# Kernel optimization log

Measured on AMD Instinct MI355X. Metric: run time of the kernel, lower is better.

## Reference

```python
import jax, jax.numpy as jnp
import numpy as np

B, L, H = 2, 2048, 2048
NH, NKV, HD = 16, 8, 128
K = 4            # conv kernel size
BASE = 1000000.0 # rotary base
H2 = NH // 2
N_REP = NH // NKV


def setup_inputs() -> dict:
    key = jax.random.key(0)
    ks = jax.random.split(key, 12)
    s = 0.02
    hidden_states = jax.random.normal(ks[0], (B, L, H), jnp.float32)
    idx = jnp.arange(L)
    diff = (idx[:, None] - idx[None, :]).astype(jnp.float32)
    # lightning-attention decay mask: -(i-j) on/below diagonal, -1e9 above
    lin_attention_mask = jnp.where(diff >= 0, -diff, -1e9).astype(jnp.float32)
    # additive causal mask for softmax half
    attention_mask = jnp.where(diff >= 0, 0.0, -1e9).astype(jnp.float32)[None, None]
    # ALiBi-style positive per-head slopes for the linear half
    slope_rate = (2.0 ** (-8.0 * jnp.arange(1, H2 + 1, dtype=jnp.float32) / H2)).reshape(H2, 1, 1)
    position_ids = jnp.arange(L, dtype=jnp.int32)
    Wq = s * jax.random.normal(ks[1], (H, H), jnp.float32)
    bq = jnp.zeros((H,), jnp.float32)
    Wk = s * jax.random.normal(ks[2], (H, NKV * HD), jnp.float32)
    bk = jnp.zeros((NKV * HD,), jnp.float32)
    Wv = s * jax.random.normal(ks[3], (H, NKV * HD), jnp.float32)
    bv = jnp.zeros((NKV * HD,), jnp.float32)
    Wo = s * jax.random.normal(ks[4], (H, H), jnp.float32)
    # conv init: identity tap at last index + tiny noise (matches _init_conv_to_one)
    q_conv_w = jnp.zeros((H // 2, K), jnp.float32).at[:, K - 1].set(1.0) + 1e-4 * jax.random.normal(ks[5], (H // 2, K), jnp.float32)
    q_conv_b = jnp.zeros((H // 2,), jnp.float32)
    k_conv_w = jnp.zeros((NKV * HD, K), jnp.float32).at[:, K - 1].set(1.0) + 1e-4 * jax.random.normal(ks[6], (NKV * HD, K), jnp.float32)
    k_conv_b = jnp.zeros((NKV * HD,), jnp.float32)
    return dict(hidden_states=hidden_states, lin_attention_mask=lin_attention_mask,
                attention_mask=attention_mask, slope_rate=slope_rate, position_ids=position_ids,
                Wq=Wq, bq=bq, Wk=Wk, bk=bk, Wv=Wv, bv=bv, Wo=Wo,
                q_conv_w=q_conv_w, q_conv_b=q_conv_b, k_conv_w=k_conv_w, k_conv_b=k_conv_b)


def _dwconv_causal(x, w, b):
    # x: [B,L,C]; w: [C,K]; b: [C]. Causal depthwise conv (torch Conv1d cross-correlation,
    # padding K-1 then truncate to first L positions).
    xp = jnp.pad(x, ((0, 0), (K - 1, 0), (0, 0)))
    y = b
    for i in range(K):
        y = y + xp[:, i:i + x.shape[1], :] * w[:, i]
    return y


def _rot_half(x):
    return jnp.concatenate([-x[..., HD // 2:], x[..., :HD // 2]], axis=-1)


def _rep_kv(x):
    # [B,NKV,L,D] -> [B,NH,L,D] via repeat_interleave on head dim
    return jnp.repeat(x, N_REP, axis=1)


def reference(hidden_states, lin_attention_mask, attention_mask, slope_rate, position_ids,
              Wq, bq, Wk, bk, Wv, bv, Wo, q_conv_w, q_conv_b, k_conv_w, k_conv_b):
    q = hidden_states @ Wq + bq          # [B,L,H]
    k = hidden_states @ Wk + bk          # [B,L,NKV*HD]
    v = hidden_states @ Wv + bv          # [B,L,NKV*HD]

    # ---- softmax half (first NH//2 heads, rotary) ----
    qs = q[..., :H // 2].reshape(B, L, H2, HD).transpose(0, 2, 1, 3)   # [B,H2,L,D]
    ks_ = k.reshape(B, L, NKV, HD).transpose(0, 2, 1, 3)               # [B,NKV,L,D]
    vs = v.reshape(B, L, NKV, HD).transpose(0, 2, 1, 3)
    inv_freq = 1.0 / (BASE ** (jnp.arange(0, HD, 2, dtype=jnp.float32) / HD))
    freqs = position_ids.astype(jnp.float32)[:, None] * inv_freq[None, :]
    emb = jnp.concatenate([freqs, freqs], axis=-1)                     # [L,D]
    cos, sin = jnp.cos(emb)[None, None], jnp.sin(emb)[None, None]
    qs = qs * cos + _rot_half(qs) * sin
    kr = ks_ * cos + _rot_half(ks_) * sin
    k_soft = _rep_kv(kr)[:, :H2]
    v_soft = _rep_kv(vs)[:, :H2]
    attn = jnp.einsum('bhnd,bhmd->bhnm', qs, k_soft) / np.sqrt(HD).astype(np.float32)
    attn = attn + attention_mask
    attn = jax.nn.softmax(attn.astype(jnp.float32), axis=-1).astype(qs.dtype)
    attn_out = jnp.einsum('bhnm,bhmd->bhnd', attn, v_soft)
    attn_out = attn_out.transpose(0, 2, 1, 3).reshape(B, L, H // 2)

    # ---- linear half (last NH//2 heads: conv -> silu -> decayed linear attention) ----
    q_tnorm = _dwconv_causal(q[..., H // 2:], q_conv_w, q_conv_b)      # [B,L,H/2]
    kc = _dwconv_causal(k, k_conv_w, k_conv_b)                          # [B,L,NKV*HD]
    qt = jax.nn.silu(q_tnorm).reshape(B, L, H2, HD).transpose(0, 2, 1, 3)
    kc = jax.nn.silu(kc).reshape(B, L, NKV, HD).transpose(0, 2, 1, 3)
    k_lin = _rep_kv(kc)[:, H2:]
    v_lin = _rep_kv(vs)[:, H2:]
    lin_mask = jnp.exp(slope_rate * lin_attention_mask)                 # [H2,L,L]
    energy = jnp.einsum('bhnd,bhmd->bhnm', qt, k_lin) * lin_mask
    out_t = jnp.einsum('bhnm,bhmd->bhnd', energy, v_lin)
    out_t = out_t.transpose(0, 2, 1, 3).reshape(B, L, H // 2)
    # SimpleRMSNorm (no weight), computed in fp32
    ot32 = out_t.astype(jnp.float32)
    out_t = (ot32 * jax.lax.rsqrt(jnp.mean(ot32 * ot32, axis=-1, keepdims=True) + 1e-6)).astype(out_t.dtype)

    return jnp.concatenate([attn_out, out_t], axis=-1) @ Wo
```

## Files before the change

kernel.cpp:

```cpp
#include <hip/hip_runtime.h>
#include <hip/hip_bf16.h>

typedef __attribute__((ext_vector_type(8))) short short8;
typedef __attribute__((ext_vector_type(4))) float f32x4;
typedef __attribute__((ext_vector_type(16))) float f32x16;

__device__ __forceinline__ void gl_lds16(const void* g, void* l) {
    void* gp = const_cast<void*>(g);
    __builtin_amdgcn_global_load_lds((__attribute__((address_space(1))) void*)gp,
                                     (__attribute__((address_space(3))) void*)l, 16, 0, 0);
}
__device__ __forceinline__ short f2bf(float f) {
    __hip_bfloat16 h = __float2bfloat16(f);
    return __builtin_bit_cast(short, h);
}
__device__ __forceinline__ float bf2f(__hip_bfloat16 h) { return __bfloat162float(h); }
__device__ __forceinline__ float bfbits2f(short s) {
    unsigned int u = ((unsigned int)(unsigned short)s) << 16;
    return __builtin_bit_cast(float, u);
}
__device__ __forceinline__ void store_val(float* C, size_t i, float v) { C[i] = v; }
__device__ __forceinline__ void store_val(__hip_bfloat16* C, size_t i, float v) { C[i] = __float2bfloat16(v); }

__global__ __launch_bounds__(256) void cast_kernel(const float* __restrict__ in, __hip_bfloat16* __restrict__ out) {
    size_t i = (size_t)blockIdx.x * 256 + threadIdx.x;
    float4 v = ((const float4*)in)[i];
    ushort4 o;
    o.x = (unsigned short)f2bf(v.x); o.y = (unsigned short)f2bf(v.y);
    o.z = (unsigned short)f2bf(v.z); o.w = (unsigned short)f2bf(v.w);
    ((ushort4*)out)[i] = o;
}

__global__ __launch_bounds__(256) void biascat_kernel(const float* __restrict__ bq, const float* __restrict__ bk,
                                                      const float* __restrict__ bv, float* __restrict__ o) {
    int i = blockIdx.x * 256 + threadIdx.x;
    o[i] = (i < 2048) ? bq[i] : ((i < 3072) ? bk[i - 2048] : bv[i - 3072]);
}

__global__ __launch_bounds__(256) void transpose_w4_kernel(
    const float* __restrict__ Wq, const float* __restrict__ Wo,
    const float* __restrict__ Wk, const float* __restrict__ Wv,
    __hip_bfloat16* __restrict__ oq, __hip_bfloat16* __restrict__ oo, __hip_bfloat16* __restrict__ okv)
{
    int z = blockIdx.z;
    const float* in; __hip_bfloat16* out; int C;
    if (z == 0)      { in = Wq; out = oq; C = 2048; }
    else if (z == 1) { in = Wo; out = oo; C = 2048; }
    else if (z == 2) { in = Wk; out = okv; C = 1024; }
    else             { in = Wv; out = okv + (size_t)1024 * 2048; C = 1024; }
    int c0 = blockIdx.x * 64, r0 = blockIdx.y * 64;
    if (c0 >= C) return;
    __shared__ float tile[64][65];
    int t = threadIdx.x, tx = t & 15, ty = t >> 4;
#pragma unroll
    for (int i = 0; i < 4; ++i) {
        float4 v = *(const float4*)(in + (size_t)(r0 + ty + i * 16) * C + c0 + tx * 4);
        tile[ty + i * 16][tx * 4 + 0] = v.x; tile[ty + i * 16][tx * 4 + 1] = v.y;
        tile[ty + i * 16][tx * 4 + 2] = v.z; tile[ty + i * 16][tx * 4 + 3] = v.w;
    }
    __syncthreads();
#pragma unroll
    for (int i = 0; i < 4; ++i) {
        int lc = ty + i * 16, lr0 = tx * 4;
        ushort4 o;
        o.x = (unsigned short)f2bf(tile[lr0 + 0][lc]);
        o.y = (unsigned short)f2bf(tile[lr0 + 1][lc]);
        o.z = (unsigned short)f2bf(tile[lr0 + 2][lc]);
        o.w = (unsigned short)f2bf(tile[lr0 + 3][lc]);
        *(ushort4*)(out + (size_t)(c0 + lc) * 2048 + r0 + lr0) = o;
    }
}

template <typename OutT, bool HAS_BIAS, bool SPLIT>
__global__ __launch_bounds__(256) void gemm_bt_kernel(
    const __hip_bfloat16* __restrict__ A, const __hip_bfloat16* __restrict__ Bt,
    const float* __restrict__ bias, OutT* __restrict__ C, OutT* __restrict__ C2,
    int M, int N, int K)
{
    __shared__ short As[128 * 64];
    __shared__ short Bs[128 * 64];
    int t = threadIdx.x, lane = t & 63, w = t >> 6;
    int m0 = blockIdx.y * 128, n0 = blockIdx.x * 128;
    int wr = (w >> 1) * 64, wc = (w & 1) * 64;
    f32x16 acc[2][2];
#pragma unroll
    for (int i = 0; i < 2; ++i)
#pragma unroll
        for (int j = 0; j < 2; ++j)
#pragma unroll
            for (int e = 0; e < 16; ++e) acc[i][j][e] = 0.f;
    int srow = w * 8 + (lane >> 3);
    int scol = ((lane & 7) ^ (lane >> 3)) * 8;
    const __hip_bfloat16* Ag = A + (size_t)(m0 + srow) * K + scol;
    const __hip_bfloat16* Bg = Bt + (size_t)(n0 + srow) * K + scol;
    short* AsB = As + w * 8 * 64;
    short* BsB = Bs + w * 8 * 64;
    int l31 = lane & 31, khalf = lane >> 5;
    for (int k0 = 0; k0 < K; k0 += 64) {
#pragma unroll
        for (int it = 0; it < 4; ++it) {
            gl_lds16(Ag + (size_t)it * 32 * K + k0, AsB + it * 32 * 64);
            gl_lds16(Bg + (size_t)it * 32 * K + k0, BsB + it * 32 * 64);
        }
        __syncthreads();
#pragma unroll
        for (int s = 0; s < 4; ++s) {
            int chunk = s * 2 + khalf;
            short8 a[2], b[2];
#pragma unroll
            for (int mi = 0; mi < 2; ++mi) {
                int row = wr + mi * 32 + l31;
                a[mi] = *(const short8*)&As[row * 64 + ((chunk ^ (row & 7)) * 8)];
            }
#pragma unroll
            for (int ni = 0; ni < 2; ++ni) {
                int row = wc + ni * 32 + l31;
                b[ni] = *(const short8*)&Bs[row * 64 + ((chunk ^ (row & 7)) * 8)];
            }
#pragma unroll
            for (int mi = 0; mi < 2; ++mi)
#pragma unroll
                for (int ni = 0; ni < 2; ++ni)
                    acc[mi][ni] = __builtin_amdgcn_mfma_f32_32x32x16_bf16(a[mi], b[ni], acc[mi][ni], 0, 0, 0);
        }
        __syncthreads();
    }
    bool hi = SPLIT && (n0 + wc) >= 2048;
    OutT* Cw = hi ? C2 : C;
    int nbase = SPLIT ? ((n0 + wc) - (hi ? 2048 : 0)) : (n0 + wc);
    int Nw = SPLIT ? 2048 : N;
#pragma unroll
    for (int ni = 0; ni < 2; ++ni) {
        float bias_v = HAS_BIAS ? bias[n0 + wc + ni * 32 + l31] : 0.f;
        int n = nbase + ni * 32 + l31;
#pragma unroll
        for (int mi = 0; mi < 2; ++mi) {
#pragma unroll
            for (int reg = 0; reg < 16; ++reg) {
                int m = m0 + wr + mi * 32 + (reg & 3) + 8 * (reg >> 2) + 4 * khalf;
                store_val(Cw, (size_t)m * Nw + n, acc[mi][ni][reg] + bias_v);
            }
        }
    }
}

__global__ __launch_bounds__(256) void prepq_kernel(const __hip_bfloat16* __restrict__ qf, const int* __restrict__ pid,
                                                    const float* __restrict__ w, const float* __restrict__ bias,
                                                    __hip_bfloat16* __restrict__ Qs, __hip_bfloat16* __restrict__ qt) {
    size_t idx = (size_t)blockIdx.x * 256 + threadIdx.x;
    int c = idx & 2047; int l = (int)((idx >> 11) & 2047); int b = (int)(idx >> 22);
    size_t row = (size_t)(b * 2048 + l) * 2048;
    if (c < 1024) {
        int h = c >> 7, d = c & 127, j = d & 63;
        float posv = (float)pid[l];
        float ang = posv * expf(-0.21586735246819178f * (float)j);
        float cs = cosf(ang), sn = sinf(ang);
        float x = bf2f(qf[row + c]);
        float xr = (d < 64) ? -bf2f(qf[row + c + 64]) : bf2f(qf[row + c - 64]);
        Qs[(((size_t)(b * 8 + h) * 2048) + l) * 128 + d] = __float2bfloat16(x * cs + xr * sn);
    } else {
        int ch = c - 1024;
        float y = bias[ch];
#pragma unroll
        for (int i = 0; i < 4; ++i) {
            int ls = l - 3 + i;
            if (ls >= 0) y += w[ch * 4 + i] * bf2f(qf[(size_t)(b * 2048 + ls) * 2048 + 1024 + ch]);
        }
        y = y / (1.f + __expf(-y));
        qt[(((size_t)(b * 8 + (ch >> 7)) * 2048) + l) * 128 + (ch & 127)] = __float2bfloat16(y);
    }
}

__global__ __launch_bounds__(256) void prepk_kernel(const __hip_bfloat16* __restrict__ kvf, const int* __restrict__ pid,
                                                    const float* __restrict__ w, const float* __restrict__ bias,
                                                    __hip_bfloat16* __restrict__ Ks, __hip_bfloat16* __restrict__ kc) {
    size_t idx = (size_t)blockIdx.x * 256 + threadIdx.x;
    int cc = idx & 1023; int l = (int)((idx >> 10) & 2047); int b = (int)(idx >> 21);
    size_t row = (size_t)(b * 2048 + l) * 2048;
    if (cc < 512) {
        int kvh = cc >> 7, d = cc & 127, j = d & 63;
        float posv = (float)pid[l];
        float ang = posv * expf(-0.21586735246819178f * (float)j);
        float cs = cosf(ang), sn = sinf(ang);
        float x = bf2f(kvf[row + cc]);
        float xr = (d < 64) ? -bf2f(kvf[row + cc + 64]) : bf2f(kvf[row + cc - 64]);
        Ks[(((size_t)(b * 4 + kvh) * 2048) + l) * 128 + d] = __float2bfloat16(x * cs + xr * sn);
    } else {
        float y = bias[cc];
#pragma unroll
        for (int i = 0; i < 4; ++i) {
            int ls = l - 3 + i;
            if (ls >= 0) y += w[cc * 4 + i] * bf2f(kvf[(size_t)(b * 2048 + ls) * 2048 + cc]);
        }
        y = y / (1.f + __expf(-y));
        kc[(((size_t)(b * 4 + ((cc - 512) >> 7)) * 2048) + l) * 128 + (cc & 127)] = __float2bfloat16(y);
    }
}

__global__ __launch_bounds__(256) void transpose_v_kernel(const __hip_bfloat16* __restrict__ kvf, __hip_bfloat16* __restrict__ Vt) {
    __shared__ __hip_bfloat16 tile[32][33];
    int l0 = blockIdx.x * 32, d0 = blockIdx.y * 32, bh = blockIdx.z;
    int b = bh >> 3, kvh = bh & 7;
    int tx = threadIdx.x, ty = threadIdx.y;
#pragma unroll
    for (int i = 0; i < 4; ++i)
        tile[ty + i*8][tx] = kvf[(size_t)(b * 2048 + l0 + ty + i*8) * 2048 + 1024 + kvh * 128 + d0 + tx];
    __syncthreads();
#pragma unroll
    for (int i = 0; i < 4; ++i)
        Vt[(size_t)(bh * 128 + d0 + ty + i*8) * 2048 + l0 + tx] = tile[tx][ty + i*8];
}

__device__ __forceinline__ float redsum16(float v) {
    v += __shfl_xor(v, 1); v += __shfl_xor(v, 2);
    v += __shfl_xor(v, 4); v += __shfl_xor(v, 8);
    return v;
}
__device__ __forceinline__ void decode_slice(int x, int& q, int& jl, int& jh) {
    int sub;
    if (x < 8)       { q = x; sub = 0; }
    else if (x < 24) { q = 8 + ((x - 8) >> 1); sub = (x - 8) & 1; }
    else if (x < 48) { int u = x - 24; int d = u / 3; q = 16 + d; sub = u - 3 * d; }
    else             { int u = x - 48; q = 24 + (u >> 2); sub = u & 3; }
    jl = sub * 8;
    jh = min(jl + 8, q + 1);
}
__device__ __forceinline__ int slice_base(int q) {
    if (q < 8)  return q;
    if (q < 16) return 8 + 2 * (q - 8);
    if (q < 24) return 24 + 3 * (q - 16);
    return 48 + 4 * (q - 24);
}

__global__ __launch_bounds__(256, 4) void flash_part_kernel(
    const __hip_bfloat16* __restrict__ Qs, const __hip_bfloat16* __restrict__ Ks,
    const __hip_bfloat16* __restrict__ Vt, __hip_bfloat16* __restrict__ partO, float* __restrict__ partL)
{
    __shared__ short Kt[64 * 128];
    __shared__ short Vl[128 * 64];
    __shared__ short Pl[4][16 * 64];
    int x = blockIdx.x, bh = blockIdx.y;
    int q, jl, jh; decode_slice(x, q, jl, jh);
    int b = bh >> 3, h = bh & 7;
    int t = threadIdx.x, lane = t & 63, w = t >> 6, quad = lane >> 4, c0 = lane & 15;
    const __hip_bfloat16* Qrow = Qs + ((size_t)(b * 8 + h) * 2048 + q * 64 + w * 16 + c0) * 128;
    short8 qa[4];
#pragma unroll
    for (int kk = 0; kk < 4; ++kk) qa[kk] = *(const short8*)(Qrow + kk * 32 + quad * 8);
    const char* Kg = (const char*)(Ks + ((size_t)(b * 4 + (h >> 1)) * 2048) * 128);
    const __hip_bfloat16* Vg = Vt + (size_t)(b * 8 + (h >> 1)) * 128 * 2048;
    int rk = t >> 4, ck = (t & 15) ^ rk;
    int rv = t >> 3, cv = (t & 7) ^ (rv & 7);
    f32x4 O[8];
#pragma unroll
    for (int v = 0; v < 8; ++v) O[v] = (f32x4){0.f, 0.f, 0.f, 0.f};
    float lacc[4] = {0.f, 0.f, 0.f, 0.f};
    const float scale = 0.08838834764831845f;
    int gi0 = q * 64 + w * 16;
    for (int j0 = jl; j0 < jh; ++j0) {
#pragma unroll
        for (int it = 0; it < 4; ++it) {
            gl_lds16(Kg + (size_t)(j0 * 64 + it * 16 + rk) * 256 + ck * 16, (char*)Kt + it * 4096 + w * 1024);
            gl_lds16((const char*)(Vg + (size_t)(it * 32 + rv) * 2048 + j0 * 64 + cv * 8), (char*)Vl + it * 4096 + w * 1024);
        }
        __syncthreads();
        f32x4 S[4];
#pragma unroll
        for (int ni = 0; ni < 4; ++ni) S[ni] = (f32x4){0.f, 0.f, 0.f, 0.f};
#pragma unroll
        for (int kk = 0; kk < 4; ++kk) {
#pragma unroll
            for (int ni = 0; ni < 4; ++ni) {
                short8 bb = *(const short8*)&Kt[(ni * 16 + c0) * 128 + (((kk * 4 + quad) ^ c0) * 8)];
                S[ni] = __builtin_amdgcn_mfma_f32_16x16x32_bf16(qa[kk], bb, S[ni], 0, 0, 0);
            }
        }
        bool diag = (j0 == q);
#pragma unroll
        for (int ni = 0; ni < 4; ++ni) {
            int gj = j0 * 64 + ni * 16 + c0;
#pragma unroll
            for (int r = 0; r < 4; ++r) {
                int gi = gi0 + quad * 4 + r;
                float p = (diag && gj > gi) ? 0.f : __expf(S[ni][r] * scale);
                lacc[r] += p;
                int m = quad * 4 + r;
                Pl[w][m * 64 + (((ni * 2 + (c0 >> 3)) ^ (m & 7)) * 8) + (c0 & 7)] = f2bf(p);
            }
        }
#pragma unroll
        for (int kk = 0; kk < 2; ++kk) {
            short8 a = *(const short8*)&Pl[w][c0 * 64 + (((kk * 4 + quad) ^ (c0 & 7)) * 8)];
#pragma unroll
            for (int v = 0; v < 8; ++v) {
                short8 bb = *(const short8*)&Vl[(v * 16 + c0) * 64 + (((kk * 4 + quad) ^ (c0 & 7)) * 8)];
                O[v] = __builtin_amdgcn_mfma_f32_16x16x32_bf16(a, bb, O[v], 0, 0, 0);
            }
        }
        __syncthreads();
    }
#pragma unroll
    for (int r = 0; r < 4; ++r) {
        float lr = redsum16(lacc[r]);
        if (c0 == 0) partL[((size_t)(bh * 80 + x)) * 64 + w * 16 + quad * 4 + r] = lr;
    }
    size_t pb = (size_t)(bh * 80 + x) * 64 * 128;
#pragma unroll
    for (int v = 0; v < 8; ++v)
#pragma unroll
        for (int r = 0; r < 4; ++r)
            partO[pb + (size_t)(w * 16 + quad * 4 + r) * 128 + v * 16 + c0] = __float2bfloat16(O[v][r]);
}

__global__ __launch_bounds__(256) void flash_merge_kernel(const __hip_bfloat16* __restrict__ partO, const float* __restrict__ partL,
                                                          __hip_bfloat16* __restrict__ CC) {
    int q = blockIdx.x, bh = blockIdx.y, b = bh >> 3, h = bh & 7;
    int t = threadIdx.x, row = t >> 2, cg = (t & 3) * 32;
    int base = slice_base(q), ns = (q + 8) >> 3;
    float lt = 0.f;
    float acc[32];
#pragma unroll
    for (int i = 0; i < 32; ++i) acc[i] = 0.f;
    for (int s = 0; s < ns; ++s) {
        size_t sb = (size_t)(bh * 80 + base + s);
        lt += partL[sb * 64 + row];
        const short* po = (const short*)partO + (sb * 64 + row) * 128 + cg;
#pragma unroll
        for (int g = 0; g < 4; ++g) {
            short8 vv = *(const short8*)(po + g * 8);
#pragma unroll
            for (int e = 0; e < 8; ++e) acc[g * 8 + e] += bfbits2f(vv[e]);
        }
    }
    float inv = 1.f / lt;
    __hip_bfloat16* co = CC + ((size_t)(b * 2048 + q * 64 + row)) * 2048 + h * 128 + cg;
#pragma unroll
    for (int g = 0; g < 4; ++g) {
        short8 o;
#pragma unroll
        for (int e = 0; e < 8; ++e) o[e] = f2bf(acc[g * 8 + e] * inv);
        *(short8*)(co + g * 8) = o;
    }
}

__global__ __launch_bounds__(256, 4) void lin_part_kernel(
    const __hip_bfloat16* __restrict__ Qb, const __hip_bfloat16* __restrict__ Kb,
    const __hip_bfloat16* __restrict__ Vt, const float* __restrict__ slope, __hip_bfloat16* __restrict__ partO)
{
    __shared__ short Kt[64 * 128];
    __shared__ short Vl[128 * 64];
    __shared__ short Pl[4][16 * 64];
    int x = blockIdx.x, bh = blockIdx.y;
    int q, jl, jh; decode_slice(x, q, jl, jh);
    int b = bh >> 3, hh = bh & 7;
    float s = slope[hh];
    float thr = ((float)(q * 64) - 63.f - 25.f / s) * (1.f / 64.f);
    int jlo = thr > 0.f ? (int)ceilf(thr) : 0;
    if (jlo > q) jlo = q;
    int jstart = max(jl, jlo);
    if (jstart >= jh) return;
    int t = threadIdx.x, lane = t & 63, w = t >> 6, quad = lane >> 4, c0 = lane & 15;
    const __hip_bfloat16* Qrow = Qb + ((size_t)(b * 8 + hh) * 2048 + q * 64 + w * 16 + c0) * 128;
    short8 qa[4];
#pragma unroll
    for (int kk = 0; kk < 4; ++kk) qa[kk] = *(const short8*)(Qrow + kk * 32 + quad * 8);
    const char* Kg = (const char*)(Kb + ((size_t)(b * 4 + (hh >> 1)) * 2048) * 128);
    const __hip_bfloat16* Vg = Vt + (size_t)(b * 8 + 4 + (hh >> 1)) * 128 * 2048;
    int rk = t >> 4, ck = (t & 15) ^ rk;
    int rv = t >> 3, cv = (t & 7) ^ (rv & 7);
    f32x4 O[8];
#pragma unroll
    for (int v = 0; v < 8; ++v) O[v] = (f32x4){0.f, 0.f, 0.f, 0.f};
    int gi0 = q * 64 + w * 16;
    for (int j0 = jstart; j0 < jh; ++j0) {
#pragma unroll
        for (int it = 0; it < 4; ++it) {
            gl_lds16(Kg + (size_t)(j0 * 64 + it * 16 + rk) * 256 + ck * 16, (char*)Kt + it * 4096 + w * 1024);
            gl_lds16((const char*)(Vg + (size_t)(it * 32 + rv) * 2048 + j0 * 64 + cv * 8), (char*)Vl + it * 4096 + w * 1024);
        }
        __syncthreads();
        f32x4 S[4];
#pragma unroll
        for (int ni = 0; ni < 4; ++ni) S[ni] = (f32x4){0.f, 0.f, 0.f, 0.f};
#pragma unroll
        for (int kk = 0; kk < 4; ++kk) {
#pragma unroll
            for (int ni = 0; ni < 4; ++ni) {
                short8 bb = *(const short8*)&Kt[(ni * 16 + c0) * 128 + (((kk * 4 + quad) ^ c0) * 8)];
                S[ni] = __builtin_amdgcn_mfma_f32_16x16x32_bf16(qa[kk], bb, S[ni], 0, 0, 0);
            }
        }
        bool diag = (j0 == q);
#pragma unroll
        for (int ni = 0; ni < 4; ++ni) {
            int gj = j0 * 64 + ni * 16 + c0;
#pragma unroll
            for (int r = 0; r < 4; ++r) {
                int gi = gi0 + quad * 4 + r;
                float p = 0.f;
                if (!diag || gj <= gi) p = S[ni][r] * __expf(s * (float)(gj - gi));
                int m = quad * 4 + r;
                Pl[w][m * 64 + (((ni * 2 + (c0 >> 3)) ^ (m & 7)) * 8) + (c0 & 7)] = f2bf(p);
            }
        }
#pragma unroll
        for (int kk = 0; kk < 2; ++kk) {
            short8 a = *(const short8*)&Pl[w][c0 * 64 + (((kk * 4 + quad) ^ (c0 & 7)) * 8)];
#pragma unroll
            for (int v = 0; v < 8; ++v) {
                short8 bb = *(const short8*)&Vl[(v * 16 + c0) * 64 + (((kk * 4 + quad) ^ (c0 & 7)) * 8)];
                O[v] = __builtin_amdgcn_mfma_f32_16x16x32_bf16(a, bb, O[v], 0, 0, 0);
            }
        }
        __syncthreads();
    }
    size_t pb = (size_t)(bh * 80 + x) * 64 * 128;
#pragma unroll
    for (int v = 0; v < 8; ++v)
#pragma unroll
        for (int r = 0; r < 4; ++r)
            partO[pb + (size_t)(w * 16 + quad * 4 + r) * 128 + v * 16 + c0] = __float2bfloat16(O[v][r]);
}

__global__ __launch_bounds__(256) void lin_merge_rms_kernel(const __hip_bfloat16* __restrict__ partO, const float* __restrict__ slope,
                                                            __hip_bfloat16* __restrict__ CC) {
    int q = blockIdx.x, rg = blockIdx.y, b = blockIdx.z;
    int t = threadIdx.x;
    int row = rg * 16 + (t >> 4);
    int seg = t & 15;
    int hh = seg >> 1;
    int cs = (seg & 1) * 64;
    int bh = b * 8 + hh;
    int base = slice_base(q), ns = (q + 8) >> 3;
    float s = slope[hh];
    float thr = ((float)(q * 64) - 63.f - 25.f / s) * (1.f / 64.f);
    int jlo = thr > 0.f ? (int)ceilf(thr) : 0;
    if (jlo > q) jlo = q;
    float acc[64];
#pragma unroll
    for (int i = 0; i < 64; ++i) acc[i] = 0.f;
    for (int s_ = 0; s_ < ns; ++s_) {
        int jl2 = s_ * 8, jh2 = min(jl2 + 8, q + 1);
        if (max(jl2, jlo) >= jh2) continue;
        const short* po = (const short*)partO + ((size_t)(bh * 80 + base + s_) * 64 + row) * 128 + hh * 0 + cs;
#pragma unroll
        for (int g = 0; g < 8; ++g) {
            short8 vv = *(const short8*)(po + g * 8);
#pragma unroll
            for (int e = 0; e < 8; ++e) acc[g * 8 + e] += bfbits2f(vv[e]);
        }
    }
    float ss = 0.f;
#pragma unroll
    for (int i = 0; i < 64; ++i) ss += acc[i] * acc[i];
    ss = redsum16(ss);
    float rs = rsqrtf(ss * (1.f / 1024.f) + 1e-6f);
    __hip_bfloat16* co = CC + ((size_t)(b * 2048 + q * 64 + row)) * 2048 + 1024 + hh * 128 + cs;
#pragma unroll
    for (int g = 0; g < 8; ++g) {
        short8 o;
#pragma unroll
        for (int e = 0; e < 8; ++e) o[e] = f2bf(acc[g * 8 + e] * rs);
        *(short8*)(co + g * 8) = o;
    }
}

extern "C" void kernel_launch(void* const* d_in, const int* in_sizes, int n_in,
                              void* d_out, int out_size, void* d_ws, size_t ws_size,
                              hipStream_t stream) {
    const float* hs   = (const float*)d_in[0];
    const float* slope= (const float*)d_in[3];
    const int*   pid  = (const int*)d_in[4];
    const float* Wq   = (const float*)d_in[5];
    const float* bq   = (const float*)d_in[6];
    const float* Wk   = (const float*)d_in[7];
    const float* bk   = (const float*)d_in[8];
    const float* Wv   = (const float*)d_in[9];
    const float* bv   = (const float*)d_in[10];
    const float* Wo   = (const float*)d_in[11];
    const float* qcw  = (const float*)d_in[12];
    const float* qcb  = (const float*)d_in[13];
    const float* kcw  = (const float*)d_in[14];
    const float* kcb  = (const float*)d_in[15];
    float* out = (float*)d_out;

    char* p = (char*)d_ws;
    auto alloc = [&](size_t bytes) { char* r = p; p += (bytes + 255) & ~(size_t)255; return r; };
    __hip_bfloat16* hsb   = (__hip_bfloat16*)alloc((size_t)4096 * 2048 * 2);
    __hip_bfloat16* bWqT  = (__hip_bfloat16*)alloc((size_t)2048 * 2048 * 2);
    __hip_bfloat16* bWkvT = (__hip_bfloat16*)alloc((size_t)2048 * 2048 * 2);
    __hip_bfloat16* bWoT  = (__hip_bfloat16*)alloc((size_t)2048 * 2048 * 2);
    float*          bqkv  = (float*)alloc(4096 * 4);
    __hip_bfloat16* qf    = (__hip_bfloat16*)alloc((size_t)4096 * 2048 * 2);
    __hip_bfloat16* kvf   = (__hip_bfloat16*)alloc((size_t)4096 * 2048 * 2);
    __hip_bfloat16* Qsb   = (__hip_bfloat16*)alloc((size_t)2 * 8 * 2048 * 128 * 2);
    __hip_bfloat16* Ksb   = (__hip_bfloat16*)alloc((size_t)2 * 4 * 2048 * 128 * 2);
    __hip_bfloat16* Vtb   = (__hip_bfloat16*)alloc((size_t)2 * 8 * 128 * 2048 * 2);
    __hip_bfloat16* qtb   = (__hip_bfloat16*)alloc((size_t)2 * 8 * 2048 * 128 * 2);
    __hip_bfloat16* kcbuf = (__hip_bfloat16*)alloc((size_t)2 * 4 * 2048 * 128 * 2);
    __hip_bfloat16* CC    = (__hip_bfloat16*)alloc((size_t)4096 * 2048 * 2);

    __hip_bfloat16* partO = (__hip_bfloat16*)qf;
    float*          partL = (float*)((char*)kvf + (size_t)8 * 1024 * 1024);

    cast_kernel<<<8192, 256, 0, stream>>>(hs, hsb);
    biascat_kernel<<<16, 256, 0, stream>>>(bq, bk, bv, bqkv);
    transpose_w4_kernel<<<dim3(32, 32, 4), 256, 0, stream>>>(Wq, Wo, Wk, Wv, bWqT, bWoT, bWkvT);

    gemm_bt_kernel<__hip_bfloat16, true, true><<<dim3(32, 32), 256, 0, stream>>>(
        hsb, bWqT, bqkv, qf, kvf, 4096, 4096, 2048);

    prepq_kernel<<<32768, 256, 0, stream>>>(qf, pid, qcw, qcb, Qsb, qtb);
    prepk_kernel<<<16384, 256, 0, stream>>>(kvf, pid, kcw, kcb, Ksb, kcbuf);
    transpose_v_kernel<<<dim3(64, 4, 16), dim3(32, 8), 0, stream>>>(kvf, Vtb);

    flash_part_kernel<<<dim3(80, 16), 256, 0, stream>>>(Qsb, Ksb, Vtb, partO, partL);
    flash_merge_kernel<<<dim3(32, 16), 256, 0, stream>>>(partO, partL, CC);
    lin_part_kernel<<<dim3(80, 16), 256, 0, stream>>>(qtb, kcbuf, Vtb, slope, partO);
    lin_merge_rms_kernel<<<dim3(32, 4, 2), 256, 0, stream>>>(partO, slope, CC);

    gemm_bt_kernel<float, false, false><<<dim3(16, 32), 256, 0, stream>>>(
        CC, bWoT, nullptr, out, nullptr, 4096, 2048, 2048);
}
```

Measured before the change: 461.6 us.

## Merge launches into fused pre, prep, attention and merge kernels; retile output GEMM

Collapses the three setup kernels into one pre_kernel, the three q/k/v prep kernels into one prep_kernel, and the softmax and linear attention part and merge kernels into single launches that dispatch on block index. Attention partials for the two halves now go to separate scratch buffers (hsb and qf) so both halves can run concurrently. The output projection GEMM switches to a 64x128 tile, giving twice as many blocks. The aim is fewer launch gaps and better load balance and occupancy on the small grids, at the cost of branchy kernels whose shared memory and registers are sized for the largest branch.

```diff
diff --git a/kernel.cpp b/kernel.cpp
--- a/kernel.cpp
+++ b/kernel.cpp
@@ -22,59 +22,60 @@
 __device__ __forceinline__ void store_val(float* C, size_t i, float v) { C[i] = v; }
 __device__ __forceinline__ void store_val(__hip_bfloat16* C, size_t i, float v) { C[i] = __float2bfloat16(v); }
 
-__global__ __launch_bounds__(256) void cast_kernel(const float* __restrict__ in, __hip_bfloat16* __restrict__ out) {
-    size_t i = (size_t)blockIdx.x * 256 + threadIdx.x;
-    float4 v = ((const float4*)in)[i];
-    ushort4 o;
-    o.x = (unsigned short)f2bf(v.x); o.y = (unsigned short)f2bf(v.y);
-    o.z = (unsigned short)f2bf(v.z); o.w = (unsigned short)f2bf(v.w);
-    ((ushort4*)out)[i] = o;
-}
-
-__global__ __launch_bounds__(256) void biascat_kernel(const float* __restrict__ bq, const float* __restrict__ bk,
-                                                      const float* __restrict__ bv, float* __restrict__ o) {
-    int i = blockIdx.x * 256 + threadIdx.x;
-    o[i] = (i < 2048) ? bq[i] : ((i < 3072) ? bk[i - 2048] : bv[i - 3072]);
-}
-
-__global__ __launch_bounds__(256) void transpose_w4_kernel(
+__global__ __launch_bounds__(256) void pre_kernel(
+    const float* __restrict__ hs, __hip_bfloat16* __restrict__ hsb,
+    const float* __restrict__ bq, const float* __restrict__ bk, const float* __restrict__ bv,
+    float* __restrict__ bqkv,
     const float* __restrict__ Wq, const float* __restrict__ Wo,
     const float* __restrict__ Wk, const float* __restrict__ Wv,
     __hip_bfloat16* __restrict__ oq, __hip_bfloat16* __restrict__ oo, __hip_bfloat16* __restrict__ okv)
 {
-    int z = blockIdx.z;
-    const float* in; __hip_bfloat16* out; int C;
-    if (z == 0)      { in = Wq; out = oq; C = 2048; }
-    else if (z == 1) { in = Wo; out = oo; C = 2048; }
-    else if (z == 2) { in = Wk; out = okv; C = 1024; }
-    else             { in = Wv; out = okv + (size_t)1024 * 2048; C = 1024; }
-    int c0 = blockIdx.x * 64, r0 = blockIdx.y * 64;
-    if (c0 >= C) return;
     __shared__ float tile[64][65];
-    int t = threadIdx.x, tx = t & 15, ty = t >> 4;
-#pragma unroll
-    for (int i = 0; i < 4; ++i) {
-        float4 v = *(const float4*)(in + (size_t)(r0 + ty + i * 16) * C + c0 + tx * 4);
-        tile[ty + i * 16][tx * 4 + 0] = v.x; tile[ty + i * 16][tx * 4 + 1] = v.y;
-        tile[ty + i * 16][tx * 4 + 2] = v.z; tile[ty + i * 16][tx * 4 + 3] = v.w;
-    }
-    __syncthreads();
-#pragma unroll
-    for (int i = 0; i < 4; ++i) {
-        int lc = ty + i * 16, lr0 = tx * 4;
+    int bx = blockIdx.x, t = threadIdx.x;
+    if (bx < 8192) {
+        size_t i = (size_t)bx * 256 + t;
+        float4 v = ((const float4*)hs)[i];
         ushort4 o;
-        o.x = (unsigned short)f2bf(tile[lr0 + 0][lc]);
-        o.y = (unsigned short)f2bf(tile[lr0 + 1][lc]);
-        o.z = (unsigned short)f2bf(tile[lr0 + 2][lc]);
-        o.w = (unsigned short)f2bf(tile[lr0 + 3][lc]);
-        *(ushort4*)(out + (size_t)(c0 + lc) * 2048 + r0 + lr0) = o;
-    }
-}
-
-template <typename OutT, bool HAS_BIAS, bool SPLIT>
-__global__ __launch_bounds__(256) void gemm_bt_kernel(
+        o.x = (unsigned short)f2bf(v.x); o.y = (unsigned short)f2bf(v.y);
+        o.z = (unsigned short)f2bf(v.z); o.w = (unsigned short)f2bf(v.w);
+        ((ushort4*)hsb)[i] = o;
+    } else if (bx < 8208) {
+        int i = (bx - 8192) * 256 + t;
+        bqkv[i] = (i < 2048) ? bq[i] : ((i < 3072) ? bk[i - 2048] : bv[i - 3072]);
+    } else {
+        int idx = bx - 8208;
+        int z = idx >> 10, rem = idx & 1023;
+        const float* in; __hip_bfloat16* out; int C;
+        if (z == 0)      { in = Wq; out = oq; C = 2048; }
+        else if (z == 1) { in = Wo; out = oo; C = 2048; }
+        else if (z == 2) { in = Wk; out = okv; C = 1024; }
+        else             { in = Wv; out = okv + (size_t)1024 * 2048; C = 1024; }
+        int c0 = (rem & 31) * 64, r0 = (rem >> 5) * 64;
+        if (c0 >= C) return;
+        int tx = t & 15, ty = t >> 4;
+#pragma unroll
+        for (int i = 0; i < 4; ++i) {
+            float4 v = *(const float4*)(in + (size_t)(r0 + ty + i * 16) * C + c0 + tx * 4);
+            tile[ty + i * 16][tx * 4 + 0] = v.x; tile[ty + i * 16][tx * 4 + 1] = v.y;
+            tile[ty + i * 16][tx * 4 + 2] = v.z; tile[ty + i * 16][tx * 4 + 3] = v.w;
+        }
+        __syncthreads();
+#pragma unroll
+        for (int i = 0; i < 4; ++i) {
+            int lc = ty + i * 16, lr0 = tx * 4;
+            ushort4 o;
+            o.x = (unsigned short)f2bf(tile[lr0 + 0][lc]);
+            o.y = (unsigned short)f2bf(tile[lr0 + 1][lc]);
+            o.z = (unsigned short)f2bf(tile[lr0 + 2][lc]);
+            o.w = (unsigned short)f2bf(tile[lr0 + 3][lc]);
+            *(ushort4*)(out + (size_t)(c0 + lc) * 2048 + r0 + lr0) = o;
+        }
+    }
+}
+
+__global__ __launch_bounds__(256) void gemm_qkv_kernel(
     const __hip_bfloat16* __restrict__ A, const __hip_bfloat16* __restrict__ Bt,
-    const float* __restrict__ bias, OutT* __restrict__ C, OutT* __restrict__ C2,
+    const float* __restrict__ bias, __hip_bfloat16* __restrict__ C, __hip_bfloat16* __restrict__ C2,
     int M, int N, int K)
 {
     __shared__ short As[128 * 64];
@@ -125,90 +126,152 @@
         }
         __syncthreads();
     }
-    bool hi = SPLIT && (n0 + wc) >= 2048;
-    OutT* Cw = hi ? C2 : C;
-    int nbase = SPLIT ? ((n0 + wc) - (hi ? 2048 : 0)) : (n0 + wc);
-    int Nw = SPLIT ? 2048 : N;
+    bool hi = (n0 + wc) >= 2048;
+    __hip_bfloat16* Cw = hi ? C2 : C;
+    int nbase = (n0 + wc) - (hi ? 2048 : 0);
 #pragma unroll
     for (int ni = 0; ni < 2; ++ni) {
-        float bias_v = HAS_BIAS ? bias[n0 + wc + ni * 32 + l31] : 0.f;
+        float bias_v = bias[n0 + wc + ni * 32 + l31];
         int n = nbase + ni * 32 + l31;
 #pragma unroll
         for (int mi = 0; mi < 2; ++mi) {
 #pragma unroll
             for (int reg = 0; reg < 16; ++reg) {
                 int m = m0 + wr + mi * 32 + (reg & 3) + 8 * (reg >> 2) + 4 * khalf;
-                store_val(Cw, (size_t)m * Nw + n, acc[mi][ni][reg] + bias_v);
-            }
-        }
-    }
-}
-
-__global__ __launch_bounds__(256) void prepq_kernel(const __hip_bfloat16* __restrict__ qf, const int* __restrict__ pid,
-                                                    const float* __restrict__ w, const float* __restrict__ bias,
-                                                    __hip_bfloat16* __restrict__ Qs, __hip_bfloat16* __restrict__ qt) {
-    size_t idx = (size_t)blockIdx.x * 256 + threadIdx.x;
-    int c = idx & 2047; int l = (int)((idx >> 11) & 2047); int b = (int)(idx >> 22);
-    size_t row = (size_t)(b * 2048 + l) * 2048;
-    if (c < 1024) {
-        int h = c >> 7, d = c & 127, j = d & 63;
-        float posv = (float)pid[l];
-        float ang = posv * expf(-0.21586735246819178f * (float)j);
-        float cs = cosf(ang), sn = sinf(ang);
-        float x = bf2f(qf[row + c]);
-        float xr = (d < 64) ? -bf2f(qf[row + c + 64]) : bf2f(qf[row + c - 64]);
-        Qs[(((size_t)(b * 8 + h) * 2048) + l) * 128 + d] = __float2bfloat16(x * cs + xr * sn);
+                Cw[(size_t)m * 2048 + n] = __float2bfloat16(acc[mi][ni][reg] + bias_v);
+            }
+        }
+    }
+}
+
+__global__ __launch_bounds__(256) void gemm_out_kernel(
+    const __hip_bfloat16* __restrict__ A, const __hip_bfloat16* __restrict__ Bt,
+    float* __restrict__ C, int M, int N, int K)
+{
+    __shared__ short As[64 * 64];
+    __shared__ short Bs[128 * 64];
+    int t = threadIdx.x, lane = t & 63, w = t >> 6;
+    int m0 = blockIdx.y * 64, n0 = blockIdx.x * 128;
+    f32x16 acc[2];
+#pragma unroll
+    for (int i = 0; i < 2; ++i)
+#pragma unroll
+        for (int e = 0; e < 16; ++e) acc[i][e] = 0.f;
+    int srow = w * 8 + (lane >> 3);
+    int scol = ((lane & 7) ^ (lane >> 3)) * 8;
+    const __hip_bfloat16* Ag = A + (size_t)(m0 + srow) * K + scol;
+    const __hip_bfloat16* Bg = Bt + (size_t)(n0 + srow) * K + scol;
+    short* AsB = As + w * 8 * 64;
+    short* BsB = Bs + w * 8 * 64;
+    int l31 = lane & 31, khalf = lane >> 5;
+    for (int k0 = 0; k0 < K; k0 += 64) {
+#pragma unroll
+        for (int it = 0; it < 2; ++it)
+            gl_lds16(Ag + (size_t)it * 32 * K + k0, AsB + it * 32 * 64);
+#pragma unroll
+        for (int it = 0; it < 4; ++it)
+            gl_lds16(Bg + (size_t)it * 32 * K + k0, BsB + it * 32 * 64);
+        __syncthreads();
+#pragma unroll
+        for (int s = 0; s < 4; ++s) {
+            int chunk = s * 2 + khalf;
+            short8 a[2], b;
+#pragma unroll
+            for (int mi = 0; mi < 2; ++mi) {
+                int row = mi * 32 + l31;
+                a[mi] = *(const short8*)&As[row * 64 + ((chunk ^ (row & 7)) * 8)];
+            }
+            {
+                int row = w * 32 + l31;
+                b = *(const short8*)&Bs[row * 64 + ((chunk ^ (row & 7)) * 8)];
+            }
+#pragma unroll
+            for (int mi = 0; mi < 2; ++mi)
+                acc[mi] = __builtin_amdgcn_mfma_f32_32x32x16_bf16(a[mi], b, acc[mi], 0, 0, 0);
+        }
+        __syncthreads();
+    }
+    int n = n0 + w * 32 + l31;
+#pragma unroll
+    for (int mi = 0; mi < 2; ++mi) {
+#pragma unroll
+        for (int reg = 0; reg < 16; ++reg) {
+            int m = m0 + mi * 32 + (reg & 3) + 8 * (reg >> 2) + 4 * khalf;
+            C[(size_t)m * N + n] = acc[mi][reg];
+        }
+    }
+}
+
+__global__ __launch_bounds__(256) void prep_kernel(
+    const __hip_bfloat16* __restrict__ qf, const __hip_bfloat16* __restrict__ kvf,
+    const int* __restrict__ pid,
+    const float* __restrict__ qw, const float* __restrict__ qb,
+    const float* __restrict__ kw, const float* __restrict__ kb,
+    __hip_bfloat16* __restrict__ Qs, __hip_bfloat16* __restrict__ qt,
+    __hip_bfloat16* __restrict__ Ks, __hip_bfloat16* __restrict__ kc,
+    __hip_bfloat16* __restrict__ Vt)
+{
+    __shared__ __hip_bfloat16 tile[32][33];
+    int bx = blockIdx.x, t = threadIdx.x;
+    if (bx < 32768) {
+        size_t idx = (size_t)bx * 256 + t;
+        int c = idx & 2047; int l = (int)((idx >> 11) & 2047); int b = (int)(idx >> 22);
+        size_t row = (size_t)(b * 2048 + l) * 2048;
+        if (c < 1024) {
+            int h = c >> 7, d = c & 127, j = d & 63;
+            float posv = (float)pid[l];
+            float ang = posv * expf(-0.21586735246819178f * (float)j);
+            float cs = cosf(ang), sn = sinf(ang);
+            float x = bf2f(qf[row + c]);
+            float xr = (d < 64) ? -bf2f(qf[row + c + 64]) : bf2f(qf[row + c - 64]);
+            Qs[(((size_t)(b * 8 + h) * 2048) + l) * 128 + d] = __float2bfloat16(x * cs + xr * sn);
+        } else {
+            int ch = c - 1024;
+            float y = qb[ch];
+#pragma unroll
+            for (int i = 0; i < 4; ++i) {
+                int ls = l - 3 + i;
+                if (ls >= 0) y += qw[ch * 4 + i] * bf2f(qf[(size_t)(b * 2048 + ls) * 2048 + 1024 + ch]);
+            }
+            y = y / (1.f + __expf(-y));
+            qt[(((size_t)(b * 8 + (ch >> 7)) * 2048) + l) * 128 + (ch & 127)] = __float2bfloat16(y);
+        }
+    } else if (bx < 49152) {
+        size_t idx = (size_t)(bx - 32768) * 256 + t;
+        int cc = idx & 1023; int l = (int)((idx >> 10) & 2047); int b = (int)(idx >> 21);
+        size_t row = (size_t)(b * 2048 + l) * 2048;
+        if (cc < 512) {
+            int kvh = cc >> 7, d = cc & 127, j = d & 63;
+            float posv = (float)pid[l];
+            float ang = posv * expf(-0.21586735246819178f * (float)j);
+            float cs = cosf(ang), sn = sinf(ang);
+            float x = bf2f(kvf[row + cc]);
+            float xr = (d < 64) ? -bf2f(kvf[row + cc + 64]) : bf2f(kvf[row + cc - 64]);
+            Ks[(((size_t)(b * 4 + kvh) * 2048) + l) * 128 + d] = __float2bfloat16(x * cs + xr * sn);
+        } else {
+            float y = kb[cc];
+#pragma unroll
+            for (int i = 0; i < 4; ++i) {
+                int ls = l - 3 + i;
+                if (ls >= 0) y += kw[cc * 4 + i] * bf2f(kvf[(size_t)(b * 2048 + ls) * 2048 + cc]);
+            }
+            y = y / (1.f + __expf(-y));
+            kc[(((size_t)(b * 4 + ((cc - 512) >> 7)) * 2048) + l) * 128 + (cc & 127)] = __float2bfloat16(y);
+        }
     } else {
-        int ch = c - 1024;
-        float y = bias[ch];
-#pragma unroll
-        for (int i = 0; i < 4; ++i) {
-            int ls = l - 3 + i;
-            if (ls >= 0) y += w[ch * 4 + i] * bf2f(qf[(size_t)(b * 2048 + ls) * 2048 + 1024 + ch]);
-        }
-        y = y / (1.f + __expf(-y));
-        qt[(((size_t)(b * 8 + (ch >> 7)) * 2048) + l) * 128 + (ch & 127)] = __float2bfloat16(y);
-    }
-}
-
-__global__ __launch_bounds__(256) void prepk_kernel(const __hip_bfloat16* __restrict__ kvf, const int* __restrict__ pid,
-                                                    const float* __restrict__ w, const float* __restrict__ bias,
-                                                    __hip_bfloat16* __restrict__ Ks, __hip_bfloat16* __restrict__ kc) {
-    size_t idx = (size_t)blockIdx.x * 256 + threadIdx.x;
-    int cc = idx & 1023; int l = (int)((idx >> 10) & 2047); int b = (int)(idx >> 21);
-    size_t row = (size_t)(b * 2048 + l) * 2048;
-    if (cc < 512) {
-        int kvh = cc >> 7, d = cc & 127, j = d & 63;
-        float posv = (float)pid[l];
-        float ang = posv * expf(-0.21586735246819178f * (float)j);
-        float cs = cosf(ang), sn = sinf(ang);
-        float x = bf2f(kvf[row + cc]);
-        float xr = (d < 64) ? -bf2f(kvf[row + cc + 64]) : bf2f(kvf[row + cc - 64]);
-        Ks[(((size_t)(b * 4 + kvh) * 2048) + l) * 128 + d] = __float2bfloat16(x * cs + xr * sn);
-    } else {
-        float y = bias[cc];
-#pragma unroll
-        for (int i = 0; i < 4; ++i) {
-            int ls = l - 3 + i;
-            if (ls >= 0) y += w[cc * 4 + i] * bf2f(kvf[(size_t)(b * 2048 + ls) * 2048 + cc]);
-        }
-        y = y / (1.f + __expf(-y));
-        kc[(((size_t)(b * 4 + ((cc - 512) >> 7)) * 2048) + l) * 128 + (cc & 127)] = __float2bfloat16(y);
-    }
-}
-
-__global__ __launch_bounds__(256) void transpose_v_kernel(const __hip_bfloat16* __restrict__ kvf, __hip_bfloat16* __restrict__ Vt) {
-    __shared__ __hip_bfloat16 tile[32][33];
-    int l0 = blockIdx.x * 32, d0 = blockIdx.y * 32, bh = blockIdx.z;
-    int b = bh >> 3, kvh = bh & 7;
-    int tx = threadIdx.x, ty = threadIdx.y;
-#pragma unroll
-    for (int i = 0; i < 4; ++i)
-        tile[ty + i*8][tx] = kvf[(size_t)(b * 2048 + l0 + ty + i*8) * 2048 + 1024 + kvh * 128 + d0 + tx];
-    __syncthreads();
-#pragma unroll
-    for (int i = 0; i < 4; ++i)
-        Vt[(size_t)(bh * 128 + d0 + ty + i*8) * 2048 + l0 + tx] = tile[tx][ty + i*8];
+        int idx = bx - 49152;
+        int bh = idx >> 8, rem = idx & 255;
+        int d0 = (rem >> 6) * 32, l0 = (rem & 63) * 32;
+        int b = bh >> 3, kvh = bh & 7;
+        int tx = t & 31, ty = t >> 5;
+#pragma unroll
+        for (int i = 0; i < 4; ++i)
+            tile[ty + i*8][tx] = kvf[(size_t)(b * 2048 + l0 + ty + i*8) * 2048 + 1024 + kvh * 128 + d0 + tx];
+        __syncthreads();
+#pragma unroll
+        for (int i = 0; i < 4; ++i)
+            Vt[(size_t)(bh * 128 + d0 + ty + i*8) * 2048 + l0 + tx] = tile[tx][ty + i*8];
+    }
 }
 
 __device__ __forceinline__ float redsum16(float v) {
@@ -232,31 +295,48 @@
     return 48 + 4 * (q - 24);
 }
 
-__global__ __launch_bounds__(256, 4) void flash_part_kernel(
+__global__ __launch_bounds__(256, 4) void attn_part_kernel(
     const __hip_bfloat16* __restrict__ Qs, const __hip_bfloat16* __restrict__ Ks,
-    const __hip_bfloat16* __restrict__ Vt, __hip_bfloat16* __restrict__ partO, float* __restrict__ partL)
+    const __hip_bfloat16* __restrict__ Vt,
+    const __hip_bfloat16* __restrict__ Qb, const __hip_bfloat16* __restrict__ Kb,
+    const float* __restrict__ slope,
+    __hip_bfloat16* __restrict__ partOf, float* __restrict__ partL,
+    __hip_bfloat16* __restrict__ partOl)
 {
     __shared__ short Kt[64 * 128];
     __shared__ short Vl[128 * 64];
     __shared__ short Pl[4][16 * 64];
-    int x = blockIdx.x, bh = blockIdx.y;
+    int bxr = blockIdx.x, bh = blockIdx.y;
+    int x = bxr >> 1;
+    bool is_lin = (bxr & 1);
     int q, jl, jh; decode_slice(x, q, jl, jh);
     int b = bh >> 3, h = bh & 7;
     int t = threadIdx.x, lane = t & 63, w = t >> 6, quad = lane >> 4, c0 = lane & 15;
-    const __hip_bfloat16* Qrow = Qs + ((size_t)(b * 8 + h) * 2048 + q * 64 + w * 16 + c0) * 128;
-    short8 qa[4];
-#pragma unroll
-    for (int kk = 0; kk < 4; ++kk) qa[kk] = *(const short8*)(Qrow + kk * 32 + quad * 8);
-    const char* Kg = (const char*)(Ks + ((size_t)(b * 4 + (h >> 1)) * 2048) * 128);
-    const __hip_bfloat16* Vg = Vt + (size_t)(b * 8 + (h >> 1)) * 128 * 2048;
     int rk = t >> 4, ck = (t & 15) ^ rk;
     int rv = t >> 3, cv = (t & 7) ^ (rv & 7);
+    int gi0 = q * 64 + w * 16;
+    float s = 0.f;
+    if (is_lin) {
+        s = slope[h];
+        float thr = ((float)(q * 64) - 63.f - 25.f / s) * (1.f / 64.f);
+        int jlo = thr > 0.f ? (int)ceilf(thr) : 0;
+        if (jlo > q) jlo = q;
+        if (jlo > jl) jl = jlo;
+        if (jl >= jh) return;
+    }
+    const __hip_bfloat16* Qbase = is_lin ? Qb : Qs;
+    const __hip_bfloat16* Kbase = is_lin ? Kb : Ks;
+    const __hip_bfloat16* Qrow = Qbase + ((size_t)(b * 8 + h) * 2048 + q * 64 + w * 16 + c0) * 128;
+    short8 qa[4];
+#pragma unroll
+    for (int kk = 0; kk < 4; ++kk) qa[kk] = *(const short8*)(Qrow + kk * 32 + quad * 8);
+    const char* Kg = (const char*)(Kbase + ((size_t)(b * 4 + (h >> 1)) * 2048) * 128);
+    const __hip_bfloat16* Vg = Vt + (size_t)(b * 8 + (is_lin ? 4 : 0) + (h >> 1)) * 128 * 2048;
     f32x4 O[8];
 #pragma unroll
     for (int v = 0; v < 8; ++v) O[v] = (f32x4){0.f, 0.f, 0.f, 0.f};
     float lacc[4] = {0.f, 0.f, 0.f, 0.f};
     const float scale = 0.08838834764831845f;
-    int gi0 = q * 64 + w * 16;
     for (int j0 = jl; j0 < jh; ++j0) {
 #pragma unroll
         for (int it = 0; it < 4; ++it) {
@@ -276,16 +356,31 @@
             }
         }
         bool diag = (j0 == q);
-#pragma unroll
-        for (int ni = 0; ni < 4; ++ni) {
-            int gj = j0 * 64 + ni * 16 + c0;
-#pragma unroll
-            for (int r = 0; r < 4; ++r) {
-                int gi = gi0 + quad * 4 + r;
-                float p = (diag && gj > gi) ? 0.f : __expf(S[ni][r] * scale);
-                lacc[r] += p;
-                int m = quad * 4 + r;
-                Pl[w][m * 64 + (((ni * 2 + (c0 >> 3)) ^ (m & 7)) * 8) + (c0 & 7)] = f2bf(p);
+        if (!is_lin) {
+#pragma unroll
+            for (int ni = 0; ni < 4; ++ni) {
+                int gj = j0 * 64 + ni * 16 + c0;
+#pragma unroll
+                for (int r = 0; r < 4; ++r) {
+                    int gi = gi0 + quad * 4 + r;
+                    float p = (diag && gj > gi) ? 0.f : __expf(S[ni][r] * scale);
+                    lacc[r] += p;
+                    int m = quad * 4 + r;
+                    Pl[w][m * 64 + (((ni * 2 + (c0 >> 3)) ^ (m & 7)) * 8) + (c0 & 7)] = f2bf(p);
+                }
+            }
+        } else {
+#pragma unroll
+            for (int ni = 0; ni < 4; ++ni) {
+                int gj = j0 * 64 + ni * 16 + c0;
+#pragma unroll
+                for (int r = 0; r < 4; ++r) {
+                    int gi = gi0 + quad * 4 + r;
+                    float p = 0.f;
+                    if (!diag || gj <= gi) p = S[ni][r] * __expf(s * (float)(gj - gi));
+                    int m = quad * 4 + r;
+                    Pl[w][m * 64 + (((ni * 2 + (c0 >> 3)) ^ (m & 7)) * 8) + (c0 & 7)] = f2bf(p);
+                }
             }
         }
 #pragma unroll
@@ -299,169 +394,95 @@
         }
         __syncthreads();
     }
-#pragma unroll
-    for (int r = 0; r < 4; ++r) {
-        float lr = redsum16(lacc[r]);
-        if (c0 == 0) partL[((size_t)(bh * 80 + x)) * 64 + w * 16 + quad * 4 + r] = lr;
-    }
-    size_t pb = (size_t)(bh * 80 + x) * 64 * 128;
+    if (!is_lin) {
+#pragma unroll
+        for (int r = 0; r < 4; ++r) {
+            float lr = redsum16(lacc[r]);
+            if (c0 == 0) partL[((size_t)(bh * 80 + x)) * 64 + w * 16 + quad * 4 + r] = lr;
+        }
+    }
+    __hip_bfloat16* po = (is_lin ? partOl : partOf) + (size_t)(bh * 80 + x) * 64 * 128;
 #pragma unroll
     for (int v = 0; v < 8; ++v)
 #pragma unroll
         for (int r = 0; r < 4; ++r)
-            partO[pb + (size_t)(w * 16 + quad * 4 + r) * 128 + v * 16 + c0] = __float2bfloat16(O[v][r]);
-}
-
-__global__ __launch_bounds__(256) void flash_merge_kernel(const __hip_bfloat16* __restrict__ partO, const float* __restrict__ partL,
-                                                          __hip_bfloat16* __restrict__ CC) {
-    int q = blockIdx.x, bh = blockIdx.y, b = bh >> 3, h = bh & 7;
-    int t = threadIdx.x, row = t >> 2, cg = (t & 3) * 32;
-    int base = slice_base(q), ns = (q + 8) >> 3;
-    float lt = 0.f;
-    float acc[32];
-#pragma unroll
-    for (int i = 0; i < 32; ++i) acc[i] = 0.f;
-    for (int s = 0; s < ns; ++s) {
-        size_t sb = (size_t)(bh * 80 + base + s);
-        lt += partL[sb * 64 + row];
-        const short* po = (const short*)partO + (sb * 64 + row) * 128 + cg;
+            po[(size_t)(w * 16 + quad * 4 + r) * 128 + v * 16 + c0] = __float2bfloat16(O[v][r]);
+}
+
+__global__ __launch_bounds__(256) void merge_kernel(
+    const __hip_bfloat16* __restrict__ partOf, const float* __restrict__ partL,
+    const __hip_bfloat16* __restrict__ partOl, const float* __restrict__ slope,
+    __hip_bfloat16* __restrict__ CC)
+{
+    int bx = blockIdx.x, t = threadIdx.x;
+    if (bx < 512) {
+        int q = bx & 31, bh = bx >> 5, b = bh >> 3, h = bh & 7;
+        int row = t >> 2, cg = (t & 3) * 32;
+        int base = slice_base(q), ns = (q + 8) >> 3;
+        float lt = 0.f;
+        float acc[32];
+#pragma unroll
+        for (int i = 0; i < 32; ++i) acc[i] = 0.f;
+        for (int s = 0; s < ns; ++s) {
+            size_t sb = (size_t)(bh * 80 + base + s);
+            lt += partL[sb * 64 + row];
+            const short* po = (const short*)partOf + (sb * 64 + row) * 128 + cg;
+#pragma unroll
+            for (int g = 0; g < 4; ++g) {
+                short8 vv = *(const short8*)(po + g * 8);
+#pragma unroll
+                for (int e = 0; e < 8; ++e) acc[g * 8 + e] += bfbits2f(vv[e]);
+            }
+        }
+        float inv = 1.f / lt;
+        __hip_bfloat16* co = CC + ((size_t)(b * 2048 + q * 64 + row)) * 2048 + h * 128 + cg;
 #pragma unroll
         for (int g = 0; g < 4; ++g) {
-            short8 vv = *(const short8*)(po + g * 8);
-#pragma unroll
-            for (int e = 0; e < 8; ++e) acc[g * 8 + e] += bfbits2f(vv[e]);
-        }
-    }
-    float inv = 1.f / lt;
-    __hip_bfloat16* co = CC + ((size_t)(b * 2048 + q * 64 + row)) * 2048 + h * 128 + cg;
-#pragma unroll
-    for (int g = 0; g < 4; ++g) {
-        short8 o;
-#pragma unroll
-        for (int e = 0; e < 8; ++e) o[e] = f2bf(acc[g * 8 + e] * inv);
-        *(short8*)(co + g * 8) = o;
-    }
-}
-
-__global__ __launch_bounds__(256, 4) void lin_part_kernel(
-    const __hip_bfloat16* __restrict__ Qb, const __hip_bfloat16* __restrict__ Kb,
-    const __hip_bfloat16* __restrict__ Vt, const float* __restrict__ slope, __hip_bfloat16* __restrict__ partO)
-{
-    __shared__ short Kt[64 * 128];
-    __shared__ short Vl[128 * 64];
-    __shared__ short Pl[4][16 * 64];
-    int x = blockIdx.x, bh = blockIdx.y;
-    int q, jl, jh; decode_slice(x, q, jl, jh);
-    int b = bh >> 3, hh = bh & 7;
-    float s = slope[hh];
-    float thr = ((float)(q * 64) - 63.f - 25.f / s) * (1.f / 64.f);
-    int jlo = thr > 0.f ? (int)ceilf(thr) : 0;
-    if (jlo > q) jlo = q;
-    int jstart = max(jl, jlo);
-    if (jstart >= jh) return;
-    int t = threadIdx.x, lane = t & 63, w = t >> 6, quad = lane >> 4, c0 = lane & 15;
-    const __hip_bfloat16* Qrow = Qb + ((size_t)(b * 8 + hh) * 2048 + q * 64 + w * 16 + c0) * 128;
-    short8 qa[4];
-#pragma unroll
-    for (int kk = 0; kk < 4; ++kk) qa[kk] = *(const short8*)(Qrow + kk * 32 + quad * 8);
-    const char* Kg = (const char*)(Kb + ((size_t)(b * 4 + (hh >> 1)) * 2048) * 128);
-    const __hip_bfloat16* Vg = Vt + (size_t)(b * 8 + 4 + (hh >> 1)) * 128 * 2048;
-    int rk = t >> 4, ck = (t & 15) ^ rk;
-    int rv = t >> 3, cv = (t & 7) ^ (rv & 7);
-    f32x4 O[8];
-#pragma unroll
-    for (int v = 0; v < 8; ++v) O[v] = (f32x4){0.f, 0.f, 0.f, 0.f};
-    int gi0 = q * 64 + w * 16;
-    for (int j0 = jstart; j0 < jh; ++j0) {
-#pragma unroll
-        for (int it = 0; it < 4; ++it) {
-            gl_lds16(Kg + (size_t)(j0 * 64 + it * 16 + rk) * 256 + ck * 16, (char*)Kt + it * 4096 + w * 1024);
-            gl_lds16((const char*)(Vg + (size_t)(it * 32 + rv) * 2048 + j0 * 64 + cv * 8), (char*)Vl + it * 4096 + w * 1024);
-        }
-        __syncthreads();
-        f32x4 S[4];
-#pragma unroll
-        for (int ni = 0; ni < 4; ++ni) S[ni] = (f32x4){0.f, 0.f, 0.f, 0.f};
-#pragma unroll
-        for (int kk = 0; kk < 4; ++kk) {
-#pragma unroll
-            for (int ni = 0; ni < 4; ++ni) {
-                short8 bb = *(const short8*)&Kt[(ni * 16 + c0) * 128 + (((kk * 4 + quad) ^ c0) * 8)];
-                S[ni] = __builtin_amdgcn_mfma_f32_16x16x32_bf16(qa[kk], bb, S[ni], 0, 0, 0);
-            }
-        }
-        bool diag = (j0 == q);
-#pragma unroll
-        for (int ni = 0; ni < 4; ++ni) {
-            int gj = j0 * 64 + ni * 16 + c0;
-#pragma unroll
-            for (int r = 0; r < 4; ++r) {
-                int gi = gi0 + quad * 4 + r;
-                float p = 0.f;
-                if (!diag || gj <= gi) p = S[ni][r] * __expf(s * (float)(gj - gi));
-                int m = quad * 4 + r;
-                Pl[w][m * 64 + (((ni * 2 + (c0 >> 3)) ^ (m & 7)) * 8) + (c0 & 7)] = f2bf(p);
-            }
-        }
-#pragma unroll
-        for (int kk = 0; kk < 2; ++kk) {
-            short8 a = *(const short8*)&Pl[w][c0 * 64 + (((kk * 4 + quad) ^ (c0 & 7)) * 8)];
-#pragma unroll
-            for (int v = 0; v < 8; ++v) {
-                short8 bb = *(const short8*)&Vl[(v * 16 + c0) * 64 + (((kk * 4 + quad) ^ (c0 & 7)) * 8)];
-                O[v] = __builtin_amdgcn_mfma_f32_16x16x32_bf16(a, bb, O[v], 0, 0, 0);
-            }
-        }
-        __syncthreads();
-    }
-    size_t pb = (size_t)(bh * 80 + x) * 64 * 128;
-#pragma unroll
-    for (int v = 0; v < 8; ++v)
-#pragma unroll
-        for (int r = 0; r < 4; ++r)
-            partO[pb + (size_t)(w * 16 + quad * 4 + r) * 128 + v * 16 + c0] = __float2bfloat16(O[v][r]);
-}
-
-__global__ __launch_bounds__(256) void lin_merge_rms_kernel(const __hip_bfloat16* __restrict__ partO, const float* __restrict__ slope,
-                                                            __hip_bfloat16* __restrict__ CC) {
-    int q = blockIdx.x, rg = blockIdx.y, b = blockIdx.z;
-    int t = threadIdx.x;
-    int row = rg * 16 + (t >> 4);
-    int seg = t & 15;
-    int hh = seg >> 1;
-    int cs = (seg & 1) * 64;
-    int bh = b * 8 + hh;
-    int base = slice_base(q), ns = (q + 8) >> 3;
-    float s = slope[hh];
-    float thr = ((float)(q * 64) - 63.f - 25.f / s) * (1.f / 64.f);
-    int jlo = thr > 0.f ? (int)ceilf(thr) : 0;
-    if (jlo > q) jlo = q;
-    float acc[64];
-#pragma unroll
-    for (int i = 0; i < 64; ++i) acc[i] = 0.f;
-    for (int s_ = 0; s_ < ns; ++s_) {
-        int jl2 = s_ * 8, jh2 = min(jl2 + 8, q + 1);
-        if (max(jl2, jlo) >= jh2) continue;
-        const short* po = (const short*)partO + ((size_t)(bh * 80 + base + s_) * 64 + row) * 128 + hh * 0 + cs;
+            short8 o;
+#pragma unroll
+            for (int e = 0; e < 8; ++e) o[e] = f2bf(acc[g * 8 + e] * inv);
+            *(short8*)(co + g * 8) = o;
+        }
+    } else {
+        int idx = bx - 512;
+        int q = idx & 31, rg = (idx >> 5) & 3, b = idx >> 7;
+        int row = rg * 16 + (t >> 4);
+        int seg = t & 15;
+        int hh = seg >> 1;
+        int cs = (seg & 1) * 64;
+        int bh = b * 8 + hh;
+        int base = slice_base(q), ns = (q + 8) >> 3;
+        float s = slope[hh];
+        float thr = ((float)(q * 64) - 63.f - 25.f / s) * (1.f / 64.f);
+        int jlo = thr > 0.f ? (int)ceilf(thr) : 0;
+        if (jlo > q) jlo = q;
+        float acc[64];
+#pragma unroll
+        for (int i = 0; i < 64; ++i) acc[i] = 0.f;
+        for (int s_ = 0; s_ < ns; ++s_) {
+            int jl2 = s_ * 8, jh2 = min(jl2 + 8, q + 1);
+            if (max(jl2, jlo) >= jh2) continue;
+            const short* po = (const short*)partOl + ((size_t)(bh * 80 + base + s_) * 64 + row) * 128 + cs;
+#pragma unroll
+            for (int g = 0; g < 8; ++g) {
+                short8 vv = *(const short8*)(po + g * 8);
+#pragma unroll
+                for (int e = 0; e < 8; ++e) acc[g * 8 + e] += bfbits2f(vv[e]);
+            }
+        }
+        float ss = 0.f;
+#pragma unroll
+        for (int i = 0; i < 64; ++i) ss += acc[i] * acc[i];
+        ss = redsum16(ss);
+        float rs = rsqrtf(ss * (1.f / 1024.f) + 1e-6f);
+        __hip_bfloat16* co = CC + ((size_t)(b * 2048 + q * 64 + row)) * 2048 + 1024 + hh * 128 + cs;
 #pragma unroll
         for (int g = 0; g < 8; ++g) {
-            short8 vv = *(const short8*)(po + g * 8);
-#pragma unroll
-            for (int e = 0; e < 8; ++e) acc[g * 8 + e] += bfbits2f(vv[e]);
-        }
-    }
-    float ss = 0.f;
-#pragma unroll
-    for (int i = 0; i < 64; ++i) ss += acc[i] * acc[i];
-    ss = redsum16(ss);
-    float rs = rsqrtf(ss * (1.f / 1024.f) + 1e-6f);
-    __hip_bfloat16* co = CC + ((size_t)(b * 2048 + q * 64 + row)) * 2048 + 1024 + hh * 128 + cs;
-#pragma unroll
-    for (int g = 0; g < 8; ++g) {
-        short8 o;
-#pragma unroll
-        for (int e = 0; e < 8; ++e) o[e] = f2bf(acc[g * 8 + e] * rs);
-        *(short8*)(co + g * 8) = o;
+            short8 o;
+#pragma unroll
+            for (int e = 0; e < 8; ++e) o[e] = f2bf(acc[g * 8 + e] * rs);
+            *(short8*)(co + g * 8) = o;
+        }
     }
 }
 
@@ -500,25 +521,18 @@
     __hip_bfloat16* kcbuf = (__hip_bfloat16*)alloc((size_t)2 * 4 * 2048 * 128 * 2);
     __hip_bfloat16* CC    = (__hip_bfloat16*)alloc((size_t)4096 * 2048 * 2);
 
-    __hip_bfloat16* partO = (__hip_bfloat16*)qf;
-    float*          partL = (float*)((char*)kvf + (size_t)8 * 1024 * 1024);
-
-    cast_kernel<<<8192, 256, 0, stream>>>(hs, hsb);
-    biascat_kernel<<<16, 256, 0, stream>>>(bq, bk, bv, bqkv);
-    transpose_w4_kernel<<<dim3(32, 32, 4), 256, 0, stream>>>(Wq, Wo, Wk, Wv, bWqT, bWoT, bWkvT);
-
-    gemm_bt_kernel<__hip_bfloat16, true, true><<<dim3(32, 32), 256, 0, stream>>>(
-        hsb, bWqT, bqkv, qf, kvf, 4096, 4096, 2048);
-
-    prepq_kernel<<<32768, 256, 0, stream>>>(qf, pid, qcw, qcb, Qsb, qtb);
-    prepk_kernel<<<16384, 256, 0, stream>>>(kvf, pid, kcw, kcb, Ksb, kcbuf);
-    transpose_v_kernel<<<dim3(64, 4, 16), dim3(32, 8), 0, stream>>>(kvf, Vtb);
-
-    flash_part_kernel<<<dim3(80, 16), 256, 0, stream>>>(Qsb, Ksb, Vtb, partO, partL);
-    flash_merge_kernel<<<dim3(32, 16), 256, 0, stream>>>(partO, partL, CC);
-    lin_part_kernel<<<dim3(80, 16), 256, 0, stream>>>(qtb, kcbuf, Vtb, slope, partO);
-    lin_merge_rms_kernel<<<dim3(32, 4, 2), 256, 0, stream>>>(partO, slope, CC);
-
-    gemm_bt_kernel<float, false, false><<<dim3(16, 32), 256, 0, stream>>>(
-        CC, bWoT, nullptr, out, nullptr, 4096, 2048, 2048);
-}
+    __hip_bfloat16* partOf = (__hip_bfloat16*)hsb;
+    __hip_bfloat16* partOl = (__hip_bfloat16*)qf;
+    float*          partL  = (float*)((char*)kvf + (size_t)8 * 1024 * 1024);
+
+    pre_kernel<<<12304, 256, 0, stream>>>(hs, hsb, bq, bk, bv, bqkv, Wq, Wo, Wk, Wv, bWqT, bWoT, bWkvT);
+
+    gemm_qkv_kernel<<<dim3(32, 32), 256, 0, stream>>>(hsb, bWqT, bqkv, qf, kvf, 4096, 4096, 2048);
+
+    prep_kernel<<<53248, 256, 0, stream>>>(qf, kvf, pid, qcw, qcb, kcw, kcb, Qsb, qtb, Ksb, kcbuf, Vtb);
+
+    attn_part_kernel<<<dim3(160, 16), 256, 0, stream>>>(Qsb, Ksb, Vtb, qtb, kcbuf, slope, partOf, partL, partOl);
+    merge_kernel<<<768, 256, 0, stream>>>(partOf, partL, partOl, slope, CC);
+
+    gemm_out_kernel<<<dim3(16, 64), 256, 0, stream>>>(CC, bWoT, out, 4096, 2048, 2048);
+}
```

Result: faster. 429.3 us (-7.0%).
